# Performance work log

Measured on AMD Instinct MI355X. Metric: run time of the kernel, lower is better.

The kernel has to match this reference:

```python
import jax, jax.numpy as jnp
import numpy as np

N_NODES = 100000
N_EDGES = 1600000
D_IN = 128
D_H = 128
N_CLASSES = 64


def setup_inputs() -> dict:
    key = jax.random.key(0)
    ks = jax.random.split(key, 8)
    feat = jax.random.normal(ks[0], (N_NODES, D_IN), dtype=jnp.float32)
    src = jax.random.randint(ks[1], (N_EDGES,), 0, N_NODES)
    dst = jax.random.randint(ks[2], (N_EDGES,), 0, N_NODES)
    # Xavier-ish scaled weights (nn.Linear layout: [out, in])
    W1 = jax.random.normal(ks[3], (D_H, D_IN), dtype=jnp.float32) * (1.0 / np.sqrt(D_IN))
    b1 = jnp.zeros((D_H,), dtype=jnp.float32)
    W2 = jax.random.normal(ks[4], (D_H, D_H), dtype=jnp.float32) * (1.0 / np.sqrt(D_H))
    b2 = jnp.zeros((D_H,), dtype=jnp.float32)
    Wl = jax.random.normal(ks[5], (N_CLASSES, 2 * D_H), dtype=jnp.float32) * (1.0 / np.sqrt(2 * D_H))
    bl = jnp.zeros((N_CLASSES,), dtype=jnp.float32)
    return {"feat": feat, "src": src, "dst": dst, "W1": W1, "b1": b1,
            "W2": W2, "b2": b2, "Wl": Wl, "bl": bl}


def _mean_agg(h, src, dst, inv_deg, n):
    # copy_u('h','m') + mean('m','neigh'): gather src features, segment-sum on dst, divide by in-degree
    s = jax.ops.segment_sum(h[src], dst, num_segments=n)  # [N, D]
    return s * inv_deg


def reference(feat, src, dst, W1, b1, W2, b2, Wl, bl):
    n = feat.shape[0]
    deg = jax.ops.segment_sum(jnp.ones_like(dst, dtype=feat.dtype), dst, num_segments=n)
    inv_deg = (1.0 / jnp.maximum(deg, 1.0))[:, None]  # zero-degree nodes -> 0 (sum is 0 anyway)
    h1 = jax.nn.relu(_mean_agg(feat, src, dst, inv_deg, n) @ W1.T + b1)
    h2 = jax.nn.relu(_mean_agg(h1, src, dst, inv_deg, n) @ W2.T + b2)
    logits = jnp.concatenate([h1, h2], axis=-1) @ Wl.T + bl
    return jax.nn.log_softmax(logits, axis=-1)
```

## Files before the change

### kernel.cpp

```cpp
#include <hip/hip_runtime.h>
#include <hip/hip_fp8.h>
#include <stdint.h>

#define D 128
#define NCLS 64
#define BSH 7
#define NBMAX 1024
#define CCHUNK 4096

typedef __bf16 bf16x8 __attribute__((ext_vector_type(8)));
typedef float f32x4 __attribute__((ext_vector_type(4)));
typedef float f32x2 __attribute__((ext_vector_type(2)));

union B8 { uint4 u; bf16x8 v; };

__device__ __forceinline__ B8 pack8(const float4& a, const float4& b) {
  union { __bf16 h[8]; uint4 u; } p;
  p.h[0] = (__bf16)a.x; p.h[1] = (__bf16)a.y; p.h[2] = (__bf16)a.z; p.h[3] = (__bf16)a.w;
  p.h[4] = (__bf16)b.x; p.h[5] = (__bf16)b.y; p.h[6] = (__bf16)b.z; p.h[7] = (__bf16)b.w;
  B8 r; r.u = p.u; return r;
}


__global__ __launch_bounds__(256) void k_bhist(const int* __restrict__ dst,
                                               int* __restrict__ bcnt, int E, int NB) {
  __shared__ int h[NBMAX];
  for (int i = threadIdx.x; i < NB; i += 256) h[i] = 0;
  __syncthreads();
  for (int e = blockIdx.x * 256 + threadIdx.x; e < E; e += gridDim.x * 256)
    atomicAdd(&h[dst[e] >> BSH], 1);
  __syncthreads();
  for (int i = threadIdx.x; i < NB; i += 256) {
    int c = h[i];
    if (c) atomicAdd(&bcnt[i], c);
  }
}

__global__ __launch_bounds__(1024) void k_bscan(const int* __restrict__ bcnt,
                                                int* __restrict__ bbase,
                                                int* __restrict__ bcur, int NB, int E) {
  __shared__ int sm[NBMAX];
  const int tid = threadIdx.x;
  int v = (tid < NB) ? bcnt[tid] : 0;
  sm[tid] = v;
  __syncthreads();
  for (int off = 1; off < NBMAX; off <<= 1) {
    int t = (tid >= off) ? sm[tid - off] : 0;
    __syncthreads();
    sm[tid] += t;
    __syncthreads();
  }
  if (tid < NB) {
    bbase[tid] = sm[tid] - v;
    bcur[tid] = sm[tid] - v;
  }
  if (tid == 0) bbase[NB] = E;
}

__global__ __launch_bounds__(256) void k_bscatter(const int* __restrict__ src,
                                                  const int* __restrict__ dst,
                                                  int* __restrict__ bcur,
                                                  int* __restrict__ ebuck, int E, int NB) {
  __shared__ int h[NBMAX];
  __shared__ int base[NBMAX];
  const int beg = blockIdx.x * CCHUNK;
  const int end = min(beg + CCHUNK, E);
  for (int i = threadIdx.x; i < NB; i += 256) h[i] = 0;
  __syncthreads();
  for (int e = beg + threadIdx.x; e < end; e += 256)
    atomicAdd(&h[dst[e] >> BSH], 1);
  __syncthreads();
  for (int i = threadIdx.x; i < NB; i += 256) {
    int c = h[i];
    base[i] = c ? atomicAdd(&bcur[i], c) : 0;
    h[i] = 0;
  }
  __syncthreads();
  for (int e = beg + threadIdx.x; e < end; e += 256) {
    const int d = dst[e];
    const int b = d >> BSH;
    const int r = atomicAdd(&h[b], 1);
    ebuck[base[b] + r] = (src[e] << BSH) | (d & 127);
  }
}

__global__ __launch_bounds__(256) void k_bbuild(const int* __restrict__ ebuck,
                                                const int* __restrict__ bbase,
                                                int* __restrict__ row_ptr,
                                                int* __restrict__ esrc,
                                                float* __restrict__ inv, int N, int E) {
  __shared__ int cnt[128], s[128], cur[128];
  const int b = blockIdx.x;
  const int n0 = b << BSH;
  const int nn = min(128, N - n0);
  const int beg = bbase[b], end = bbase[b + 1];
  const int tid = threadIdx.x;
  if (tid < 128) cnt[tid] = 0;
  __syncthreads();
  for (int e = beg + tid; e < end; e += 256)
    atomicAdd(&cnt[ebuck[e] & 127], 1);
  __syncthreads();
  if (tid < 128) s[tid] = cnt[tid];
  __syncthreads();
  for (int off = 1; off < 128; off <<= 1) {
    int t = (tid < 128 && tid >= off) ? s[tid - off] : 0;
    __syncthreads();
    if (tid < 128) s[tid] += t;
    __syncthreads();
  }
  if (tid < 128) {
    const int ex = s[tid] - cnt[tid];
    cur[tid] = ex;
    if (tid < nn) {
      row_ptr[n0 + tid] = beg + ex;
      inv[n0 + tid] = 1.0f / fmaxf((float)cnt[tid], 1.0f);
    }
  }
  if (b == 0 && tid == 0) row_ptr[N] = E;
  __syncthreads();
  for (int e = beg + tid; e < end; e += 256) {
    const int p = ebuck[e];
    const int r = atomicAdd(&cur[p & 127], 1);
    esrc[beg + r] = p >> BSH;
  }
}


__global__ __launch_bounds__(256) void k_gemmz1(const float* __restrict__ A,
                                                const float* __restrict__ W,
                                                unsigned char* __restrict__ Z, int N) {
  const int wave = threadIdx.x >> 6;
  const int lane = threadIdx.x & 63;
  const int l15 = lane & 15;
  const int quad = lane >> 4;

  B8 bfrag[2][4];
#pragma unroll
  for (int t = 0; t < 2; ++t) {
    const int n = wave * 32 + t * 16 + l15;
    const float* wp = W + (size_t)n * D + quad * 8;
#pragma unroll
    for (int ks = 0; ks < 4; ++ks)
      bfrag[t][ks] = pack8(*reinterpret_cast<const float4*>(wp + ks * 32),
                           *reinterpret_cast<const float4*>(wp + ks * 32 + 4));
  }

  const int mtiles = (N + 15) >> 4;
  for (int mt = blockIdx.x; mt < mtiles; mt += gridDim.x) {
    const int arow = min(mt * 16 + l15, N - 1);
    const float* ap = A + (size_t)arow * D + quad * 8;
    B8 a[4];
#pragma unroll
    for (int ks = 0; ks < 4; ++ks)
      a[ks] = pack8(*reinterpret_cast<const float4*>(ap + ks * 32),
                    *reinterpret_cast<const float4*>(ap + ks * 32 + 4));
#pragma unroll
    for (int t = 0; t < 2; ++t) {
      f32x4 acc = {0.f, 0.f, 0.f, 0.f};
#pragma unroll
      for (int ks = 0; ks < 4; ++ks)
        acc = __builtin_amdgcn_mfma_f32_16x16x32_bf16(a[ks].v, bfrag[t][ks].v, acc, 0, 0, 0);
      const int col = wave * 32 + t * 16 + l15;
#pragma unroll
      for (int r = 0; r < 4; ++r) {
        const int orow = mt * 16 + quad * 4 + r;
        if (orow < N) {
          __hip_fp8_e4m3 q((float)acc[r]);
          Z[(size_t)orow * D + col] = q.__x;
        }
      }
    }
  }
}


__global__ __launch_bounds__(256) void k_gemmz2(const ushort* __restrict__ A,
                                                const float* __restrict__ W,
                                                unsigned char* __restrict__ Z, int N) {
  const int wave = threadIdx.x >> 6;
  const int lane = threadIdx.x & 63;
  const int l15 = lane & 15;
  const int quad = lane >> 4;

  B8 bfrag[2][4];
#pragma unroll
  for (int t = 0; t < 2; ++t) {
    const int n = wave * 32 + t * 16 + l15;
    const float* wp = W + (size_t)n * D + quad * 8;
#pragma unroll
    for (int ks = 0; ks < 4; ++ks)
      bfrag[t][ks] = pack8(*reinterpret_cast<const float4*>(wp + ks * 32),
                           *reinterpret_cast<const float4*>(wp + ks * 32 + 4));
  }

  const int mtiles = (N + 15) >> 4;
  for (int mt = blockIdx.x; mt < mtiles; mt += gridDim.x) {
    const int arow = min(mt * 16 + l15, N - 1);
    const ushort* ap = A + (size_t)arow * D + quad * 8;
    B8 a[4];
#pragma unroll
    for (int ks = 0; ks < 4; ++ks)
      a[ks].u = *reinterpret_cast<const uint4*>(ap + ks * 32);
#pragma unroll
    for (int t = 0; t < 2; ++t) {
      f32x4 acc = {0.f, 0.f, 0.f, 0.f};
#pragma unroll
      for (int ks = 0; ks < 4; ++ks)
        acc = __builtin_amdgcn_mfma_f32_16x16x32_bf16(a[ks].v, bfrag[t][ks].v, acc, 0, 0, 0);
      const int col = wave * 32 + t * 16 + l15;
#pragma unroll
      for (int r = 0; r < 4; ++r) {
        const int orow = mt * 16 + quad * 4 + r;
        if (orow < N) {
          __hip_fp8_e4m3 q((float)acc[r]);
          Z[(size_t)orow * D + col] = q.__x;
        }
      }
    }
  }
}


__device__ __forceinline__ void accq8(f32x2 acc[4], const uint2& u) {
  union { uint2 v; unsigned char b[8]; } t;
  t.v = u;
#pragma unroll
  for (int i = 0; i < 4; ++i) {
    __hip_fp8_e4m3 f0, f1;
    f0.__x = t.b[2 * i];
    f1.__x = t.b[2 * i + 1];
    f32x2 d;
    d.x = (float)f0;
    d.y = (float)f1;
    acc[i] += d;
  }
}

__device__ __forceinline__ void gather_acc8(const unsigned char* __restrict__ hp,
                                            const int* __restrict__ esrc,
                                            int beg, int end, f32x2 acc[4]) {
  int e = beg;
  for (; e + 3 < end; e += 4) {
    const int4 ss = *reinterpret_cast<const int4*>(esrc + e);
    const uint2 u0 = *reinterpret_cast<const uint2*>(hp + (size_t)ss.x * D);
    const uint2 u1 = *reinterpret_cast<const uint2*>(hp + (size_t)ss.y * D);
    const uint2 u2 = *reinterpret_cast<const uint2*>(hp + (size_t)ss.z * D);
    const uint2 u3 = *reinterpret_cast<const uint2*>(hp + (size_t)ss.w * D);
    accq8(acc, u0);
    accq8(acc, u1);
    accq8(acc, u2);
    accq8(acc, u3);
  }
  for (; e < end; ++e) {
    const int s0 = esrc[e];
    const uint2 u0 = *reinterpret_cast<const uint2*>(hp + (size_t)s0 * D);
    accq8(acc, u0);
  }
}


__global__ __launch_bounds__(256) void k_gather_relu(const unsigned char* __restrict__ z,
                                                     const int* __restrict__ row_ptr,
                                                     const int* __restrict__ esrc,
                                                     const float* __restrict__ inv,
                                                     const float* __restrict__ bias,
                                                     ushort* __restrict__ out, int N) {
  const int g = threadIdx.x >> 4;
  const int w = threadIdx.x & 15;
  const unsigned char* hp = z + w * 8;
  float bb[8];
  {
    const float4 x = *reinterpret_cast<const float4*>(bias + w * 8);
    const float4 y = *reinterpret_cast<const float4*>(bias + w * 8 + 4);
    bb[0] = x.x; bb[1] = x.y; bb[2] = x.z; bb[3] = x.w;
    bb[4] = y.x; bb[5] = y.y; bb[6] = y.z; bb[7] = y.w;
  }
  const int ntiles = (N + 15) >> 4;
  for (int tile = blockIdx.x; tile < ntiles; tile += gridDim.x) {
    const int node = tile * 16 + g;
    if (node >= N) continue;
    f32x2 acc[4] = {{0.f, 0.f}, {0.f, 0.f}, {0.f, 0.f}, {0.f, 0.f}};
    gather_acc8(hp, esrc, row_ptr[node], row_ptr[node + 1], acc);
    const float iv = inv[node];
    union { __bf16 b[8]; uint4 u; } p;
#pragma unroll
    for (int i = 0; i < 4; ++i) {
      p.b[i * 2 + 0] = (__bf16)fmaxf(acc[i].x * iv + bb[i * 2 + 0], 0.f);
      p.b[i * 2 + 1] = (__bf16)fmaxf(acc[i].y * iv + bb[i * 2 + 1], 0.f);
    }
    *reinterpret_cast<uint4*>(out + (size_t)node * D + w * 8) = p.u;
  }
}


__global__ __launch_bounds__(256) void k_logits(const ushort* __restrict__ h1,
                                                const ushort* __restrict__ h2,
                                                const float* __restrict__ Wl,
                                                const float* __restrict__ bl,
                                                float* __restrict__ out, int N) {
  __shared__ float L[16][NCLS + 4];
  const int wave = threadIdx.x >> 6;
  const int lane = threadIdx.x & 63;
  const int l15 = lane & 15;
  const int quad = lane >> 4;

  B8 bfragL[8];
  const int nlc = wave * 16 + l15;
  const float bbl = bl[nlc];
  {
    const float* wp = Wl + (size_t)nlc * (2 * D) + quad * 8;
#pragma unroll
    for (int ks = 0; ks < 8; ++ks)
      bfragL[ks] = pack8(*reinterpret_cast<const float4*>(wp + ks * 32),
                         *reinterpret_cast<const float4*>(wp + ks * 32 + 4));
  }

  const int mtiles = (N + 15) >> 4;
  for (int mt = blockIdx.x; mt < mtiles; mt += gridDim.x) {
    const int arow = min(mt * 16 + l15, N - 1);
    const ushort* p1 = h1 + (size_t)arow * D + quad * 8;
    const ushort* p2 = h2 + (size_t)arow * D + quad * 8;
    f32x4 acc = {0.f, 0.f, 0.f, 0.f};
    B8 a;
#pragma unroll
    for (int ks = 0; ks < 4; ++ks) {
      a.u = *reinterpret_cast<const uint4*>(p1 + ks * 32);
      acc = __builtin_amdgcn_mfma_f32_16x16x32_bf16(a.v, bfragL[ks].v, acc, 0, 0, 0);
    }
#pragma unroll
    for (int ks = 0; ks < 4; ++ks) {
      a.u = *reinterpret_cast<const uint4*>(p2 + ks * 32);
      acc = __builtin_amdgcn_mfma_f32_16x16x32_bf16(a.v, bfragL[4 + ks].v, acc, 0, 0, 0);
    }
#pragma unroll
    for (int r = 0; r < 4; ++r)
      L[quad * 4 + r][wave * 16 + l15] = acc[r] + bbl;
    __syncthreads();
#pragma unroll
    for (int r = 0; r < 4; ++r) {
      const int row = wave * 4 + r;
      float v = L[row][lane];
      float m = v;
#pragma unroll
      for (int off = 32; off > 0; off >>= 1) m = fmaxf(m, __shfl_xor(m, off));
      float e = __expf(v - m);
#pragma unroll
      for (int off = 32; off > 0; off >>= 1) e += __shfl_xor(e, off);
      const int orow = mt * 16 + row;
      if (orow < N) out[(size_t)orow * NCLS + lane] = v - m - __logf(e);
    }
    __syncthreads();
  }
}


extern "C" void kernel_launch(void* const* d_in, const int* in_sizes, int n_in,
                              void* d_out, int out_size, void* d_ws, size_t ws_size,
                              hipStream_t stream) {
  const float* feat = (const float*)d_in[0];
  const int* src = (const int*)d_in[1];
  const int* dst = (const int*)d_in[2];
  const float* W1 = (const float*)d_in[3];
  const float* b1 = (const float*)d_in[4];
  const float* W2 = (const float*)d_in[5];
  const float* b2 = (const float*)d_in[6];
  const float* Wl = (const float*)d_in[7];
  const float* bl = (const float*)d_in[8];
  float* out = (float*)d_out;

  const int N = in_sizes[0] / D;
  const int E = in_sizes[1];
  const int NB = (N + 127) >> BSH;

  float* ws = (float*)d_ws;
  float* inv = ws;
  ushort* h1b = (ushort*)(inv + N);
  ushort* h2b = h1b + (size_t)N * D;
  unsigned char* z8 = (unsigned char*)(h2b + (size_t)N * D);
  int* row_ptr = (int*)(z8 + (size_t)N * D);
  int* esrc = row_ptr + N + 1;
  int* bcnt = esrc + E;
  int* bbase = bcnt + NBMAX;
  int* bcur = bbase + NBMAX + 1;
  int* ebuck = (int*)z8;

  hipMemsetAsync(bcnt, 0, NBMAX * sizeof(int), stream);

  k_bhist<<<256, 256, 0, stream>>>(dst, bcnt, E, NB);
  k_bscan<<<1, 1024, 0, stream>>>(bcnt, bbase, bcur, NB, E);
  k_bscatter<<<(E + CCHUNK - 1) / CCHUNK, 256, 0, stream>>>(src, dst, bcur, ebuck, E, NB);
  k_bbuild<<<NB, 256, 0, stream>>>(ebuck, bbase, row_ptr, esrc, inv, N, E);

  k_gemmz1<<<2048, 256, 0, stream>>>(feat, W1, z8, N);
  k_gather_relu<<<2048, 256, 0, stream>>>(z8, row_ptr, esrc, inv, b1, h1b, N);

  k_gemmz2<<<2048, 256, 0, stream>>>(h1b, W2, z8, N);
  k_gather_relu<<<2048, 256, 0, stream>>>(z8, row_ptr, esrc, inv, b2, h2b, N);
  k_logits<<<2048, 256, 0, stream>>>(h1b, h2b, Wl, bl, out, N);
}
```

Baseline: 389.8 us.

## Replace bucketed CSR build with global-atomic counting sort; per-wave logits tiles

Replaces the two-level bucket histogram/scatter CSR construction with a per-node global atomic histogram, a three-kernel scan and an atomic scatter into esrc. It drops the intermediate bucket buffer and the second local-sort pass, but relies on heavy global atomics contention on 100k counters. Separately, the logits kernel now has each wave compute a full 16x64 tile with all of Wl held in registers, doing log_softmax with 16-lane shuffles instead of going through LDS and __syncthreads. The logits grid is also reduced. Edge order within a row becomes nondeterministic, which only affects floating-point summation order.

```diff
diff --git a/kernel.cpp b/kernel.cpp
--- a/kernel.cpp
+++ b/kernel.cpp
@@ -4,9 +4,6 @@
 
 #define D 128
 #define NCLS 64
-#define BSH 7
-#define NBMAX 1024
-#define CCHUNK 4096
 
 typedef __bf16 bf16x8 __attribute__((ext_vector_type(8)));
 typedef float f32x4 __attribute__((ext_vector_type(4)));
@@ -22,106 +19,74 @@
 }
 
 
-__global__ __launch_bounds__(256) void k_bhist(const int* __restrict__ dst,
-                                               int* __restrict__ bcnt, int E, int NB) {
-  __shared__ int h[NBMAX];
-  for (int i = threadIdx.x; i < NB; i += 256) h[i] = 0;
+__global__ __launch_bounds__(256) void k_hist(const int* __restrict__ dst,
+                                              int* __restrict__ cnt, int E) {
+  for (int e = blockIdx.x * 256 + threadIdx.x; e < E; e += gridDim.x * 256)
+    atomicAdd(&cnt[dst[e]], 1);
+}
+
+__global__ __launch_bounds__(128) void k_scan1(const int* __restrict__ cnt,
+                                               int* __restrict__ bsum, int N) {
+  const int i = blockIdx.x * 128 + threadIdx.x;
+  int v = (i < N) ? cnt[i] : 0;
+#pragma unroll
+  for (int off = 32; off > 0; off >>= 1) v += __shfl_xor(v, off);
+  __shared__ int sm[2];
+  if ((threadIdx.x & 63) == 0) sm[threadIdx.x >> 6] = v;
   __syncthreads();
-  for (int e = blockIdx.x * 256 + threadIdx.x; e < E; e += gridDim.x * 256)
-    atomicAdd(&h[dst[e] >> BSH], 1);
-  __syncthreads();
-  for (int i = threadIdx.x; i < NB; i += 256) {
-    int c = h[i];
-    if (c) atomicAdd(&bcnt[i], c);
-  }
-}
-
-__global__ __launch_bounds__(1024) void k_bscan(const int* __restrict__ bcnt,
-                                                int* __restrict__ bbase,
-                                                int* __restrict__ bcur, int NB, int E) {
-  __shared__ int sm[NBMAX];
+  if (threadIdx.x == 0) bsum[blockIdx.x] = sm[0] + sm[1];
+}
+
+__global__ __launch_bounds__(1024) void k_scan2(const int* __restrict__ bsum,
+                                                int* __restrict__ bbase, int NB) {
+  __shared__ int sm[1024];
   const int tid = threadIdx.x;
-  int v = (tid < NB) ? bcnt[tid] : 0;
+  int v = (tid < NB) ? bsum[tid] : 0;
   sm[tid] = v;
   __syncthreads();
-  for (int off = 1; off < NBMAX; off <<= 1) {
+  for (int off = 1; off < 1024; off <<= 1) {
     int t = (tid >= off) ? sm[tid - off] : 0;
     __syncthreads();
     sm[tid] += t;
     __syncthreads();
   }
-  if (tid < NB) {
-    bbase[tid] = sm[tid] - v;
-    bcur[tid] = sm[tid] - v;
-  }
-  if (tid == 0) bbase[NB] = E;
-}
-
-__global__ __launch_bounds__(256) void k_bscatter(const int* __restrict__ src,
-                                                  const int* __restrict__ dst,
-                                                  int* __restrict__ bcur,
-                                                  int* __restrict__ ebuck, int E, int NB) {
-  __shared__ int h[NBMAX];
-  __shared__ int base[NBMAX];
-  const int beg = blockIdx.x * CCHUNK;
-  const int end = min(beg + CCHUNK, E);
-  for (int i = threadIdx.x; i < NB; i += 256) h[i] = 0;
-  __syncthreads();
-  for (int e = beg + threadIdx.x; e < end; e += 256)
-    atomicAdd(&h[dst[e] >> BSH], 1);
-  __syncthreads();
-  for (int i = threadIdx.x; i < NB; i += 256) {
-    int c = h[i];
-    base[i] = c ? atomicAdd(&bcur[i], c) : 0;
-    h[i] = 0;
-  }
-  __syncthreads();
-  for (int e = beg + threadIdx.x; e < end; e += 256) {
-    const int d = dst[e];
-    const int b = d >> BSH;
-    const int r = atomicAdd(&h[b], 1);
-    ebuck[base[b] + r] = (src[e] << BSH) | (d & 127);
-  }
-}
-
-__global__ __launch_bounds__(256) void k_bbuild(const int* __restrict__ ebuck,
-                                                const int* __restrict__ bbase,
-                                                int* __restrict__ row_ptr,
-                                                int* __restrict__ esrc,
-                                                float* __restrict__ inv, int N, int E) {
-  __shared__ int cnt[128], s[128], cur[128];
+  if (tid < NB) bbase[tid] = sm[tid] - v;
+}
+
+__global__ __launch_bounds__(128) void k_scan3(const int* __restrict__ cnt,
+                                               const int* __restrict__ bbase,
+                                               int* __restrict__ row_ptr,
+                                               int* __restrict__ cur,
+                                               float* __restrict__ inv, int N, int E) {
+  __shared__ int sm[128];
   const int b = blockIdx.x;
-  const int n0 = b << BSH;
-  const int nn = min(128, N - n0);
-  const int beg = bbase[b], end = bbase[b + 1];
   const int tid = threadIdx.x;
-  if (tid < 128) cnt[tid] = 0;
-  __syncthreads();
-  for (int e = beg + tid; e < end; e += 256)
-    atomicAdd(&cnt[ebuck[e] & 127], 1);
-  __syncthreads();
-  if (tid < 128) s[tid] = cnt[tid];
+  const int i = b * 128 + tid;
+  const int c = (i < N) ? cnt[i] : 0;
+  sm[tid] = c;
   __syncthreads();
   for (int off = 1; off < 128; off <<= 1) {
-    int t = (tid < 128 && tid >= off) ? s[tid - off] : 0;
+    int t = (tid >= off) ? sm[tid - off] : 0;
     __syncthreads();
-    if (tid < 128) s[tid] += t;
+    sm[tid] += t;
     __syncthreads();
   }
-  if (tid < 128) {
-    const int ex = s[tid] - cnt[tid];
-    cur[tid] = ex;
-    if (tid < nn) {
-      row_ptr[n0 + tid] = beg + ex;
-      inv[n0 + tid] = 1.0f / fmaxf((float)cnt[tid], 1.0f);
-    }
+  if (i < N) {
+    const int r = bbase[b] + sm[tid] - c;
+    row_ptr[i] = r;
+    cur[i] = r;
+    inv[i] = 1.0f / fmaxf((float)c, 1.0f);
   }
   if (b == 0 && tid == 0) row_ptr[N] = E;
-  __syncthreads();
-  for (int e = beg + tid; e < end; e += 256) {
-    const int p = ebuck[e];
-    const int r = atomicAdd(&cur[p & 127], 1);
-    esrc[beg + r] = p >> BSH;
+}
+
+__global__ __launch_bounds__(256) void k_scatter(const int* __restrict__ src,
+                                                 const int* __restrict__ dst,
+                                                 int* __restrict__ cur,
+                                                 int* __restrict__ esrc, int E) {
+  for (int e = blockIdx.x * 256 + threadIdx.x; e < E; e += gridDim.x * 256) {
+    const int p = atomicAdd(&cur[dst[e]], 1);
+    esrc[p] = src[e];
   }
 }
 
@@ -293,63 +258,79 @@
 }
 
 
-__global__ __launch_bounds__(256) void k_logits(const ushort* __restrict__ h1,
-                                                const ushort* __restrict__ h2,
-                                                const float* __restrict__ Wl,
-                                                const float* __restrict__ bl,
-                                                float* __restrict__ out, int N) {
-  __shared__ float L[16][NCLS + 4];
-  const int wave = threadIdx.x >> 6;
+__global__ __launch_bounds__(256, 2) void k_logits(const ushort* __restrict__ h1,
+                                                   const ushort* __restrict__ h2,
+                                                   const float* __restrict__ Wl,
+                                                   const float* __restrict__ bl,
+                                                   float* __restrict__ out, int N) {
   const int lane = threadIdx.x & 63;
   const int l15 = lane & 15;
   const int quad = lane >> 4;
-
-  B8 bfragL[8];
-  const int nlc = wave * 16 + l15;
-  const float bbl = bl[nlc];
-  {
-    const float* wp = Wl + (size_t)nlc * (2 * D) + quad * 8;
+  const int wid = blockIdx.x * 4 + (threadIdx.x >> 6);
+  const int nw = gridDim.x * 4;
+
+  B8 wfrag[4][8];
+  float blv[4];
+#pragma unroll
+  for (int t = 0; t < 4; ++t) {
+    const int n = t * 16 + l15;
+    blv[t] = bl[n];
+    const float* wp = Wl + (size_t)n * (2 * D) + quad * 8;
 #pragma unroll
     for (int ks = 0; ks < 8; ++ks)
-      bfragL[ks] = pack8(*reinterpret_cast<const float4*>(wp + ks * 32),
-                         *reinterpret_cast<const float4*>(wp + ks * 32 + 4));
+      wfrag[t][ks] = pack8(*reinterpret_cast<const float4*>(wp + ks * 32),
+                           *reinterpret_cast<const float4*>(wp + ks * 32 + 4));
   }
 
   const int mtiles = (N + 15) >> 4;
-  for (int mt = blockIdx.x; mt < mtiles; mt += gridDim.x) {
+  for (int mt = wid; mt < mtiles; mt += nw) {
     const int arow = min(mt * 16 + l15, N - 1);
     const ushort* p1 = h1 + (size_t)arow * D + quad * 8;
     const ushort* p2 = h2 + (size_t)arow * D + quad * 8;
-    f32x4 acc = {0.f, 0.f, 0.f, 0.f};
-    B8 a;
+    B8 a1[4], a2[4];
 #pragma unroll
     for (int ks = 0; ks < 4; ++ks) {
-      a.u = *reinterpret_cast<const uint4*>(p1 + ks * 32);
-      acc = __builtin_amdgcn_mfma_f32_16x16x32_bf16(a.v, bfragL[ks].v, acc, 0, 0, 0);
-    }
-#pragma unroll
-    for (int ks = 0; ks < 4; ++ks) {
-      a.u = *reinterpret_cast<const uint4*>(p2 + ks * 32);
-      acc = __builtin_amdgcn_mfma_f32_16x16x32_bf16(a.v, bfragL[4 + ks].v, acc, 0, 0, 0);
-    }
-#pragma unroll
-    for (int r = 0; r < 4; ++r)
-      L[quad * 4 + r][wave * 16 + l15] = acc[r] + bbl;
-    __syncthreads();
+      a1[ks].u = *reinterpret_cast<const uint4*>(p1 + ks * 32);
+      a2[ks].u = *reinterpret_cast<const uint4*>(p2 + ks * 32);
+    }
+    f32x4 acc[4];
+#pragma unroll
+    for (int t = 0; t < 4; ++t) acc[t] = f32x4{0.f, 0.f, 0.f, 0.f};
+#pragma unroll
+    for (int ks = 0; ks < 4; ++ks)
+#pragma unroll
+      for (int t = 0; t < 4; ++t)
+        acc[t] = __builtin_amdgcn_mfma_f32_16x16x32_bf16(a1[ks].v, wfrag[t][ks].v, acc[t], 0, 0, 0);
+#pragma unroll
+    for (int ks = 0; ks < 4; ++ks)
+#pragma unroll
+      for (int t = 0; t < 4; ++t)
+        acc[t] = __builtin_amdgcn_mfma_f32_16x16x32_bf16(a2[ks].v, wfrag[t][4 + ks].v, acc[t], 0, 0, 0);
+#pragma unroll
+    for (int t = 0; t < 4; ++t)
+#pragma unroll
+      for (int r = 0; r < 4; ++r)
+        acc[t][r] += blv[t];
 #pragma unroll
     for (int r = 0; r < 4; ++r) {
-      const int row = wave * 4 + r;
-      float v = L[row][lane];
-      float m = v;
-#pragma unroll
-      for (int off = 32; off > 0; off >>= 1) m = fmaxf(m, __shfl_xor(m, off));
-      float e = __expf(v - m);
-#pragma unroll
-      for (int off = 32; off > 0; off >>= 1) e += __shfl_xor(e, off);
-      const int orow = mt * 16 + row;
-      if (orow < N) out[(size_t)orow * NCLS + lane] = v - m - __logf(e);
-    }
-    __syncthreads();
+      float m = fmaxf(fmaxf(acc[0][r], acc[1][r]), fmaxf(acc[2][r], acc[3][r]));
+#pragma unroll
+      for (int off = 8; off > 0; off >>= 1) m = fmaxf(m, __shfl_xor(m, off));
+      const float e0 = __expf(acc[0][r] - m);
+      const float e1 = __expf(acc[1][r] - m);
+      const float e2 = __expf(acc[2][r] - m);
+      const float e3 = __expf(acc[3][r] - m);
+      float s = (e0 + e1) + (e2 + e3);
+#pragma unroll
+      for (int off = 8; off > 0; off >>= 1) s += __shfl_xor(s, off);
+      const float ls = m + __logf(s);
+      const int orow = mt * 16 + quad * 4 + r;
+      if (orow < N) {
+        float* op = out + (size_t)orow * NCLS + l15;
+#pragma unroll
+        for (int t = 0; t < 4; ++t) op[t * 16] = acc[t][r] - ls;
+      }
+    }
   }
 }
 
@@ -370,7 +351,7 @@
 
   const int N = in_sizes[0] / D;
   const int E = in_sizes[1];
-  const int NB = (N + 127) >> BSH;
+  const int NB2 = (N + 127) >> 7;
 
   float* ws = (float*)d_ws;
   float* inv = ws;
@@ -379,22 +360,23 @@
   unsigned char* z8 = (unsigned char*)(h2b + (size_t)N * D);
   int* row_ptr = (int*)(z8 + (size_t)N * D);
   int* esrc = row_ptr + N + 1;
-  int* bcnt = esrc + E;
-  int* bbase = bcnt + NBMAX;
-  int* bcur = bbase + NBMAX + 1;
-  int* ebuck = (int*)z8;
-
-  hipMemsetAsync(bcnt, 0, NBMAX * sizeof(int), stream);
-
-  k_bhist<<<256, 256, 0, stream>>>(dst, bcnt, E, NB);
-  k_bscan<<<1, 1024, 0, stream>>>(bcnt, bbase, bcur, NB, E);
-  k_bscatter<<<(E + CCHUNK - 1) / CCHUNK, 256, 0, stream>>>(src, dst, bcur, ebuck, E, NB);
-  k_bbuild<<<NB, 256, 0, stream>>>(ebuck, bbase, row_ptr, esrc, inv, N, E);
+  int* cnt = esrc + E;
+  int* cur = cnt + N;
+  int* bsum = cur + N;
+  int* bbase = bsum + 1024;
+
+  hipMemsetAsync(cnt, 0, (size_t)N * sizeof(int), stream);
+  k_hist<<<1024, 256, 0, stream>>>(dst, cnt, E);
+  k_scan1<<<NB2, 128, 0, stream>>>(cnt, bsum, N);
+  k_scan2<<<1, 1024, 0, stream>>>(bsum, bbase, NB2);
+  k_scan3<<<NB2, 128, 0, stream>>>(cnt, bbase, row_ptr, cur, inv, N, E);
+  k_scatter<<<2048, 256, 0, stream>>>(src, dst, cur, esrc, E);
 
   k_gemmz1<<<2048, 256, 0, stream>>>(feat, W1, z8, N);
   k_gather_relu<<<2048, 256, 0, stream>>>(z8, row_ptr, esrc, inv, b1, h1b, N);
 
   k_gemmz2<<<2048, 256, 0, stream>>>(h1b, W2, z8, N);
   k_gather_relu<<<2048, 256, 0, stream>>>(z8, row_ptr, esrc, inv, b2, h2b, N);
-  k_logits<<<2048, 256, 0, stream>>>(h1b, h2b, Wl, bl, out, N);
-}
+
+  k_logits<<<512, 256, 0, stream>>>(h1b, h2b, Wl, bl, out, N);
+}
```

Result: slower. 499.5 us (+28.1%).
